# Kernel tuning notes

Measured on AMD Instinct MI355X. Metric: run time of the kernel, lower is better.

The kernel has to match this reference:

```python
import jax, jax.numpy as jnp
import numpy as np

B, PQ, C, NH, L, P, FF = 8, 900, 256, 8, 4, 4, 2048
SHAPES = [(100, 152), (50, 76), (25, 38), (13, 19)]
PK = sum(h * w for h, w in SHAPES)
DH = C // NH


def setup_inputs() -> dict:
    key = jax.random.key(0)
    ks = jax.random.split(key, 20)
    s = 0.02
    w = lambda i, shp: jax.random.normal(ks[i], shp, jnp.float32) * s
    starts = np.cumsum([0] + [h * wd for h, wd in SHAPES[:-1]]).astype(np.int64)
    return dict(
        query=w(0, (B, C, PQ)),
        key=w(1, (B, C, PK)),
        query_pos=jax.random.uniform(ks[2], (B, PQ, 3)),
        key_pos=jax.random.uniform(ks[3], (B, PK, 3)),
        reference_points=jax.random.uniform(ks[4], (B, PQ, L, 2)),
        W_in=w(5, (3 * C, C)), b_in=jnp.zeros(3 * C),
        W_out=w(6, (C, C)), b_out=jnp.zeros(C),
        W_off=w(7, (NH * L * P * 2, C)),
        b_off=jax.random.uniform(ks[8], (NH * L * P * 2,), minval=-1.0, maxval=1.0),
        W_aw=w(9, (NH * L * P, C)), b_aw=jnp.zeros(NH * L * P),
        W_v=w(10, (C, C)), b_v=jnp.zeros(C),
        W_o=w(11, (C, C)), b_o=jnp.zeros(C),
        W1=w(12, (FF, C)), b1=jnp.zeros(FF),
        W2=w(13, (C, FF)), b2=jnp.zeros(C),
        g1=jnp.ones(C), be1=jnp.zeros(C),
        g2=jnp.ones(C), be2=jnp.zeros(C),
        g3=jnp.ones(C), be3=jnp.zeros(C),
        spatial_shapes=np.array(SHAPES, np.int64),
        level_start_index=starts,
    )


def layer_norm(x, g, b):
    m = x.mean(-1, keepdims=True)
    v = x.var(-1, keepdims=True)
    return (x - m) * jax.lax.rsqrt(v + 1e-5) * g + b


def mha(x, W_in, b_in, W_out, b_out):
    # x: [S, B, C]; torch nn.MultiheadAttention with q=k=v=x
    S, Bn, _ = x.shape
    qkv = x @ W_in.T + b_in
    q, k, v = jnp.split(qkv, 3, axis=-1)
    to_h = lambda t: t.reshape(S, Bn, NH, DH).transpose(1, 2, 0, 3)  # [B,H,S,Dh]
    q, k, v = to_h(q), to_h(k), to_h(v)
    attn = jax.nn.softmax(jnp.einsum('bhqd,bhkd->bhqk', q, k) / np.sqrt(DH), axis=-1)
    o = jnp.einsum('bhqk,bhkd->bhqd', attn, v).transpose(2, 0, 1, 3).reshape(S, Bn, C)
    return o @ W_out.T + b_out


def ms_deform(value, loc, aw, shapes, starts):
    # value [B,PK,NH,DH], loc [B,PQ,NH,L,P,2] in [0,1], aw [B,PQ,NH,L,P]
    v = value.transpose(0, 2, 1, 3)          # [B,NH,PK,DH]
    locT = loc.transpose(0, 2, 1, 3, 4, 5)   # [B,NH,PQ,L,P,2]
    awT = aw.transpose(0, 2, 1, 3, 4)        # [B,NH,PQ,L,P]
    out = jnp.zeros((B, NH, PQ, DH), value.dtype)
    for l, (Hl, Wl) in enumerate(shapes):
        st = starts[l]
        vl = v[:, :, st:st + Hl * Wl]        # [B,NH,Hl*Wl,DH]
        x = locT[..., l, :, 0] * Wl - 0.5    # [B,NH,PQ,P]  (align_corners=False)
        y = locT[..., l, :, 1] * Hl - 0.5
        x0 = jnp.floor(x); y0 = jnp.floor(y)
        lw, lh = x - x0, y - y0
        x0i = x0.astype(jnp.int32); y0i = y0.astype(jnp.int32)

        def gather(ix, iy):
            valid = ((ix >= 0) & (ix < Wl) & (iy >= 0) & (iy < Hl)).astype(vl.dtype)
            idx = jnp.clip(iy, 0, Hl - 1) * Wl + jnp.clip(ix, 0, Wl - 1)
            g = jnp.take_along_axis(vl, idx.reshape(B, NH, -1, 1), axis=2)
            return g.reshape(B, NH, PQ, P, DH) * valid[..., None]

        samp = (gather(x0i, y0i) * ((1 - lw) * (1 - lh))[..., None]
                + gather(x0i + 1, y0i) * (lw * (1 - lh))[..., None]
                + gather(x0i, y0i + 1) * ((1 - lw) * lh)[..., None]
                + gather(x0i + 1, y0i + 1) * (lw * lh)[..., None])  # [B,NH,PQ,P,DH]
        out = out + (samp * awT[..., l, :, None]).sum(3)
    return out.transpose(0, 2, 1, 3).reshape(B, PQ, C)


def reference(query, key, query_pos, key_pos, reference_points,
              W_in, b_in, W_out, b_out, W_off, b_off, W_aw, b_aw,
              W_v, b_v, W_o, b_o, W1, b1, W2, b2,
              g1, be1, g2, be2, g3, be3,
              spatial_shapes, level_start_index):
    shapes = [tuple(int(t) for t in r) for r in np.asarray(spatial_shapes)]
    starts = [int(t) for t in np.asarray(level_start_index)]
    q = query.transpose(2, 0, 1)   # [PQ,B,C]
    k = key.transpose(2, 0, 1)     # [PK,B,C]
    # self-attention (posembeds are None in this config)
    q = layer_norm(q + mha(q, W_in, b_in, W_out, b_out), g1, be1)
    # multi-scale deformable cross-attention
    qd = q.transpose(1, 0, 2)      # [B,PQ,C]
    kf = k.transpose(1, 0, 2)      # [B,PK,C]
    value = (kf @ W_v.T + b_v).reshape(B, PK, NH, DH)
    off = (qd @ W_off.T + b_off).reshape(B, PQ, NH, L, P, 2)
    aw = jax.nn.softmax((qd @ W_aw.T + b_aw).reshape(B, PQ, NH, L * P), -1)
    aw = aw.reshape(B, PQ, NH, L, P)
    norm = jnp.asarray([[w_, h_] for (h_, w_) in shapes], jnp.float32)  # [L,2] as (W,H)
    loc = reference_points[:, :, None, :, None, :] + off / norm[None, None, None, :, None, :]
    q2 = ms_deform(value, loc, aw, shapes, starts) @ W_o.T + b_o
    q = layer_norm(q + q2.transpose(1, 0, 2), g2, be2)
    # FFN
    ff = jax.nn.relu(q @ W1.T + b1) @ W2.T + b2
    q = layer_norm(q + ff, g3, be3)
    return q.transpose(1, 2, 0)    # [B,C,PQ]
```

## Files before the change

kernel.cpp:

```cpp
#include <hip/hip_runtime.h>
#include <hip/hip_bf16.h>
#include <stdint.h>

typedef __hip_bfloat16 bf16;
typedef short bf16x8 __attribute__((ext_vector_type(8)));
typedef short s4v    __attribute__((ext_vector_type(4)));
typedef float f32x4  __attribute__((ext_vector_type(4)));

constexpr int B_  = 8;
constexpr int PQ_ = 900;
constexpr int C_  = 256;
constexpr int NH_ = 8;
constexpr int L_  = 4;
constexpr int P_  = 4;
constexpr int FF_ = 2048;
constexpr int DH_ = 32;
constexpr int PK_ = 20197;
constexpr int VLD = 960;

__device__ __forceinline__ short f2b(float f) {
    __hip_bfloat16 h = __float2bfloat16(f);
    union { __hip_bfloat16 h; short s; } u; u.h = h; return u.s;
}
__device__ __forceinline__ float b2f(short s) {
    union { short s; __hip_bfloat16 h; } u; u.s = s; return __bfloat162float(u.h);
}

template <int NF, bool DBUF, bool AF32, bool WF32, bool CF32, bool RELU>
__launch_bounds__(256)
__global__ void mfma_gemm(const void* __restrict__ Ap, const void* __restrict__ Wp,
                          const float* __restrict__ bias, void* __restrict__ Cp,
                          int Mb, int N, int K, int tilesM,
                          int ldA, int ldW, int ldC, int nbI,
                          int64_t sAo, int64_t sAi, int64_t sWo, int64_t sWi,
                          int64_t sCo, int64_t sCi, float scale)
{
    constexpr int BN  = 64 * NF;
    constexpr int LDR = 72;
    constexpr int NB  = DBUF ? 2 : 1;
    __shared__ short As[NB * 64 * LDR];
    __shared__ short Ws[NB * BN * LDR];

    const int tid   = threadIdx.x;
    const int batch = blockIdx.y / tilesM;
    const int m0    = (blockIdx.y % tilesM) * 64;
    const int n0    = blockIdx.x * BN;
    const int outer = batch / nbI, inner = batch % nbI;
    const int64_t offA = (int64_t)outer * sAo + (int64_t)inner * sAi;
    const int64_t offW = (int64_t)outer * sWo + (int64_t)inner * sWi;
    const int64_t offC = (int64_t)outer * sCo + (int64_t)inner * sCi;

    const int w = tid >> 6, lane = tid & 63;
    const int quad = lane >> 4, lrow = lane & 15;
    const int colbase = n0 + w * 16 * NF;

    const int sm  = tid >> 2;
    const int skb = (tid & 3) * 16;

    const int T = (K + 63) / 64;

    bf16x8 areg[2];
    bf16x8 wreg[2 * NF];

    auto stageA = [&](int t) {
        const int k0 = t * 64;
        const int gm = m0 + sm;
#pragma unroll
        for (int c = 0; c < 2; ++c) {
            const int k = k0 + skb + c * 8;
            bf16x8 pk = {0, 0, 0, 0, 0, 0, 0, 0};
            if (gm < Mb && k + 8 <= K) {
                if (AF32) {
                    const float* s = (const float*)Ap + offA + (int64_t)gm * ldA + k;
                    float4 u0 = *(const float4*)s;
                    float4 u1 = *(const float4*)(s + 4);
                    pk = (bf16x8){f2b(u0.x), f2b(u0.y), f2b(u0.z), f2b(u0.w),
                                  f2b(u1.x), f2b(u1.y), f2b(u1.z), f2b(u1.w)};
                } else {
                    pk = *(const bf16x8*)((const short*)Ap + offA + (int64_t)gm * ldA + k);
                }
            }
            areg[c] = pk;
        }
    };
    auto stageW = [&](int t) {
        const int k0 = t * 64;
#pragma unroll
        for (int j = 0; j < NF; ++j) {
            const int gn = n0 + j * 64 + sm;
#pragma unroll
            for (int c = 0; c < 2; ++c) {
                const int k = k0 + skb + c * 8;
                bf16x8 pk = {0, 0, 0, 0, 0, 0, 0, 0};
                if (gn < N && k + 8 <= K) {
                    if (WF32) {
                        const float* s = (const float*)Wp + offW + (int64_t)gn * ldW + k;
                        float4 u0 = *(const float4*)s;
                        float4 u1 = *(const float4*)(s + 4);
                        pk = (bf16x8){f2b(u0.x), f2b(u0.y), f2b(u0.z), f2b(u0.w),
                                      f2b(u1.x), f2b(u1.y), f2b(u1.z), f2b(u1.w)};
                    } else {
                        pk = *(const bf16x8*)((const short*)Wp + offW + (int64_t)gn * ldW + k);
                    }
                }
                wreg[j * 2 + c] = pk;
            }
        }
    };
    auto writeLDS = [&](int buf) {
#pragma unroll
        for (int c = 0; c < 2; ++c)
            *(bf16x8*)&As[(buf * 64 + sm) * LDR + skb + c * 8] = areg[c];
#pragma unroll
        for (int j = 0; j < NF; ++j)
#pragma unroll
            for (int c = 0; c < 2; ++c)
                *(bf16x8*)&Ws[(buf * BN + j * 64 + sm) * LDR + skb + c * 8] = wreg[j * 2 + c];
    };

    f32x4 acc[4][NF];
#pragma unroll
    for (int i = 0; i < 4; ++i)
#pragma unroll
        for (int j = 0; j < NF; ++j) acc[i][j] = (f32x4){0.f, 0.f, 0.f, 0.f};

    auto compute = [&](int buf) {
        bf16x8 a[4][2], bb[NF][2];
#pragma unroll
        for (int kh = 0; kh < 2; ++kh) {
#pragma unroll
            for (int mf = 0; mf < 4; ++mf)
                a[mf][kh] = *(const bf16x8*)&As[(buf * 64 + mf * 16 + lrow) * LDR + kh * 32 + quad * 8];
#pragma unroll
            for (int nf = 0; nf < NF; ++nf)
                bb[nf][kh] = *(const bf16x8*)&Ws[(buf * BN + w * 16 * NF + nf * 16 + lrow) * LDR + kh * 32 + quad * 8];
        }
#pragma unroll
        for (int kh = 0; kh < 2; ++kh)
#pragma unroll
            for (int mf = 0; mf < 4; ++mf)
#pragma unroll
                for (int nf = 0; nf < NF; ++nf)
                    acc[mf][nf] = __builtin_amdgcn_mfma_f32_16x16x32_bf16(a[mf][kh], bb[nf][kh], acc[mf][nf], 0, 0, 0);
    };

    if (DBUF) {
        stageA(0); stageW(0); writeLDS(0);
        __syncthreads();
        for (int t = 0; t < T; ++t) {
            const int cur = t & 1;
            if (t + 1 < T) { stageA(t + 1); stageW(t + 1); }
            compute(cur);
            if (t + 1 < T) {
                writeLDS(cur ^ 1);
                __syncthreads();
            }
        }
    } else {
        for (int t = 0; t < T; ++t) {
            stageA(t); stageW(t);
            if (t > 0) __syncthreads();
            writeLDS(0);
            __syncthreads();
            compute(0);
        }
    }

#pragma unroll
    for (int nf = 0; nf < NF; ++nf) {
        const int col = colbase + nf * 16 + lrow;
        if (col >= N) continue;
        const float bia = bias ? bias[col] : 0.f;
#pragma unroll
        for (int mf = 0; mf < 4; ++mf) {
            const int row0 = m0 + mf * 16 + quad * 4;
#pragma unroll
            for (int r = 0; r < 4; ++r) {
                const int rr = row0 + r;
                if (rr < Mb) {
                    float v = acc[mf][nf][r] * scale + bia;
                    if (RELU) v = fmaxf(v, 0.f);
                    const int64_t idx = offC + (int64_t)rr * ldC + col;
                    if (CF32) ((float*)Cp)[idx] = v;
                    else      ((short*)Cp)[idx] = f2b(v);
                }
            }
        }
    }
}

template <int NF, bool DBUF, bool AF32, bool WF32, bool CF32, bool RELU>
static void mfma_launch(const void* A, const void* W, const float* bias, void* Cp,
                        int nb, int nbI, int Mb, int N, int K,
                        int ldA, int ldW, int ldC,
                        int64_t sAo, int64_t sAi, int64_t sWo, int64_t sWi,
                        int64_t sCo, int64_t sCi, float scale, hipStream_t stream)
{
    int tilesM = (Mb + 63) / 64;
    dim3 grid((N + 64 * NF - 1) / (64 * NF), nb * tilesM);
    mfma_gemm<NF, DBUF, AF32, WF32, CF32, RELU><<<grid, 256, 0, stream>>>(
        A, W, bias, Cp, Mb, N, K, tilesM, ldA, ldW, ldC, nbI,
        sAo, sAi, sWo, sWi, sCo, sCi, scale);
}

__launch_bounds__(256)
__global__ void transpose_kernel(const float* __restrict__ src, short* __restrict__ dst,
                                 int Scount, int ldS, int64_t sbs, int64_t dbs)
{
    const int tid = threadIdx.x;
    const int b = blockIdx.z;
    const int s0 = blockIdx.x * 32, c0 = blockIdx.y * 32;
    __shared__ float t[32][33];
    {
        const int c_l = tid >> 3, sq = (tid & 7) * 4;
        const int64_t base = (int64_t)b * sbs + (int64_t)(c0 + c_l) * ldS;
#pragma unroll
        for (int i = 0; i < 4; ++i) {
            const int s = s0 + sq + i;
            t[c_l][sq + i] = (s < Scount) ? src[base + s] : 0.f;
        }
    }
    __syncthreads();
    {
        const int s_l = tid >> 3, cq = (tid & 7) * 4;
        const int s = s0 + s_l;
        if (s < Scount) {
            s4v pk = {f2b(t[cq + 0][s_l]), f2b(t[cq + 1][s_l]),
                      f2b(t[cq + 2][s_l]), f2b(t[cq + 3][s_l])};
            *(s4v*)&dst[(int64_t)b * dbs + (int64_t)s * 256 + c0 + cq] = pk;
        }
    }
}

__launch_bounds__(256)
__global__ void vt_kernel(const short* __restrict__ qkv, short* __restrict__ VT)
{
    const int tid = threadIdx.x;
    const int bh = blockIdx.y, b = bh >> 3, h = bh & 7;
    const int s0 = blockIdx.x * 32;
    __shared__ short t[32][36];
    {
        const int s_l = tid >> 3, dq = (tid & 7) * 4;
        const int s = s0 + s_l;
        s4v pk = {0, 0, 0, 0};
        if (s < 900)
            pk = *(const s4v*)&qkv[((int64_t)(b * 900 + s)) * 768 + 512 + h * 32 + dq];
        *(s4v*)&t[s_l][dq] = pk;
    }
    __syncthreads();
    {
        const int d = tid >> 3, sq = (tid & 7) * 4;
        s4v pk = {t[sq + 0][d], t[sq + 1][d], t[sq + 2][d], t[sq + 3][d]};
        *(s4v*)&VT[((int64_t)bh * 32 + d) * VLD + s0 + sq] = pk;
    }
}

__launch_bounds__(256)
__global__ void attn_fused(const short* __restrict__ qkv, const short* __restrict__ VT,
                           short* __restrict__ attno)
{
    __shared__ short Pl[4 * 16 * 72];
    const int tid = threadIdx.x;
    const int wv = tid >> 6, lane = tid & 63;
    const int quad = lane >> 4, lrow = lane & 15;
    const int bh = blockIdx.y, b = bh >> 3, h = bh & 7;
    const int q0 = blockIdx.x * 64 + wv * 16;
    const float iscale = 0.17677669529663687f;

    bf16x8 aq = {0, 0, 0, 0, 0, 0, 0, 0};
    {
        const int q = q0 + lrow;
        if (q < 900)
            aq = *(const bf16x8*)&qkv[((int64_t)(b * 900 + q)) * 768 + h * 32 + quad * 8];
    }

    float mrow[4], lsum[4];
    f32x4 o[2] = {{0.f, 0.f, 0.f, 0.f}, {0.f, 0.f, 0.f, 0.f}};
#pragma unroll
    for (int r = 0; r < 4; ++r) { mrow[r] = -1e30f; lsum[r] = 0.f; }

    short* Pw = &Pl[wv * 16 * 72];

    for (int st = 0; st < 15; ++st) {
        const int s0 = st * 64;
        f32x4 sc[4];
#pragma unroll
        for (int nf = 0; nf < 4; ++nf) {
            const int s = s0 + nf * 16 + lrow;
            bf16x8 kb = {0, 0, 0, 0, 0, 0, 0, 0};
            if (s < 900)
                kb = *(const bf16x8*)&qkv[((int64_t)(b * 900 + s)) * 768 + 256 + h * 32 + quad * 8];
            sc[nf] = __builtin_amdgcn_mfma_f32_16x16x32_bf16(aq, kb, (f32x4){0.f, 0.f, 0.f, 0.f}, 0, 0, 0);
        }
#pragma unroll
        for (int nf = 0; nf < 4; ++nf) {
            const int s = s0 + nf * 16 + lrow;
            if (s >= 900) sc[nf] = (f32x4){-1e30f, -1e30f, -1e30f, -1e30f};
            else {
#pragma unroll
                for (int r = 0; r < 4; ++r) sc[nf][r] *= iscale;
            }
        }
        float alpha[4], ps[4][4], rsum[4];
#pragma unroll
        for (int r = 0; r < 4; ++r) {
            float tm = fmaxf(fmaxf(sc[0][r], sc[1][r]), fmaxf(sc[2][r], sc[3][r]));
#pragma unroll
            for (int off = 1; off < 16; off <<= 1)
                tm = fmaxf(tm, __shfl_xor(tm, off, 64));
            const float nm = fmaxf(mrow[r], tm);
            alpha[r] = __expf(mrow[r] - nm);
            mrow[r] = nm;
            float s4 = 0.f;
#pragma unroll
            for (int nf = 0; nf < 4; ++nf) {
                const float p = __expf(sc[nf][r] - nm);
                ps[nf][r] = p;
                s4 += p;
            }
#pragma unroll
            for (int off = 1; off < 16; off <<= 1)
                s4 += __shfl_xor(s4, off, 64);
            rsum[r] = s4;
        }
#pragma unroll
        for (int nf2 = 0; nf2 < 2; ++nf2)
#pragma unroll
            for (int r = 0; r < 4; ++r) o[nf2][r] *= alpha[r];
#pragma unroll
        for (int r = 0; r < 4; ++r) lsum[r] = lsum[r] * alpha[r] + rsum[r];
#pragma unroll
        for (int nf = 0; nf < 4; ++nf)
#pragma unroll
            for (int r = 0; r < 4; ++r)
                Pw[(quad * 4 + r) * 72 + nf * 16 + lrow] = f2b(ps[nf][r]);
#pragma unroll
        for (int kh = 0; kh < 2; ++kh) {
            bf16x8 pa = *(const bf16x8*)&Pw[lrow * 72 + kh * 32 + quad * 8];
#pragma unroll
            for (int nf2 = 0; nf2 < 2; ++nf2) {
                const int d = nf2 * 16 + lrow;
                bf16x8 vb = *(const bf16x8*)&VT[((int64_t)bh * 32 + d) * VLD + s0 + kh * 32 + quad * 8];
                o[nf2] = __builtin_amdgcn_mfma_f32_16x16x32_bf16(pa, vb, o[nf2], 0, 0, 0);
            }
        }
    }
#pragma unroll
    for (int r = 0; r < 4; ++r) {
        const int q = q0 + quad * 4 + r;
        if (q < 900) {
            const float inv = 1.f / lsum[r];
#pragma unroll
            for (int nf2 = 0; nf2 < 2; ++nf2)
                attno[((int64_t)(b * 900 + q)) * 256 + h * 32 + nf2 * 16 + lrow] = f2b(o[nf2][r] * inv);
        }
    }
}

template <int MODE>
__launch_bounds__(256)
__global__ void ln_kernel(const float* __restrict__ y, const void* __restrict__ res,
                          const float* __restrict__ g, const float* __restrict__ be,
                          float* __restrict__ out_f, short* __restrict__ out_b)
{
    const int bt = blockIdx.x;
    const int b = bt / PQ_, t = bt % PQ_;
    const int c = threadIdx.x;

    float r;
    if (MODE == 0)      r = ((const float*)res)[((int64_t)b * C_ + c) * PQ_ + t];
    else if (MODE == 1) r = ((const float*)res)[(int64_t)bt * C_ + c];
    else                r = b2f(((const short*)res)[(int64_t)bt * C_ + c]);
    const float v = r + y[(int64_t)bt * C_ + c];

    __shared__ float s1[256], s2[256];
    s1[c] = v; s2[c] = v * v;
    __syncthreads();
    for (int st = 128; st > 0; st >>= 1) {
        if (c < st) { s1[c] += s1[c + st]; s2[c] += s2[c + st]; }
        __syncthreads();
    }
    const float mean = s1[0] * (1.f / C_);
    const float var  = s2[0] * (1.f / C_) - mean * mean;
    const float o = (v - mean) * rsqrtf(var + 1e-5f) * g[c] + be[c];

    if (MODE == 0) { out_f[(int64_t)bt * C_ + c] = o; out_b[(int64_t)bt * C_ + c] = f2b(o); }
    else if (MODE == 1) out_b[(int64_t)bt * C_ + c] = f2b(o);
    else out_f[((int64_t)b * C_ + c) * PQ_ + t] = o;
}

__launch_bounds__(256)
__global__ void deform_kernel(const float* __restrict__ offb, const float* __restrict__ awl,
                              const float* __restrict__ refp, const short* __restrict__ value,
                              short* __restrict__ samp)
{
    const int bt = blockIdx.x;
    const int b = bt / PQ_;
    const int tid = threadIdx.x;
    const int h = tid >> 5, d = tid & 31;

    __shared__ float Loff[256];
    __shared__ float Law[128];
    __shared__ float Lref[8];

    Loff[tid] = offb[(int64_t)bt * 256 + tid];
    if (tid < 128) Law[tid] = awl[(int64_t)bt * 128 + tid];
    if (tid < 8)   Lref[tid] = refp[(int64_t)bt * 8 + tid];
    __syncthreads();

    float m = -1e30f;
#pragma unroll
    for (int i = 0; i < 16; ++i) m = fmaxf(m, Law[h * 16 + i]);
    float s = 0.f;
#pragma unroll
    for (int i = 0; i < 16; ++i) s += __expf(Law[h * 16 + i] - m);
    const float invs = 1.f / s;

    const int HLc[4] = {100, 50, 25, 13};
    const int WLc[4] = {152, 76, 38, 19};
    const int STc[4] = {0, 15200, 19000, 19950};

    float acc = 0.f;
#pragma unroll
    for (int l = 0; l < L_; ++l) {
        const int Hl = HLc[l], Wl = WLc[l], st0 = STc[l];
        const float fx = Lref[l * 2 + 0], fy = Lref[l * 2 + 1];
#pragma unroll
        for (int p = 0; p < P_; ++p) {
            const float ox = Loff[h * 32 + l * 8 + p * 2 + 0];
            const float oy = Loff[h * 32 + l * 8 + p * 2 + 1];
            const float x = (fx + ox / (float)Wl) * (float)Wl - 0.5f;
            const float y = (fy + oy / (float)Hl) * (float)Hl - 0.5f;
            const float x0f = floorf(x), y0f = floorf(y);
            const int x0 = (int)x0f, y0 = (int)y0f;
            const float lw = x - x0f, lh = y - y0f;
            const float w00 = (1.f - lw) * (1.f - lh), w10 = lw * (1.f - lh);
            const float w01 = (1.f - lw) * lh,         w11 = lw * lh;
            const float aww = __expf(Law[h * 16 + l * 4 + p] - m) * invs;

            float sv = 0.f;
            int ix, iy; float w;
#pragma unroll
            for (int cidx = 0; cidx < 4; ++cidx) {
                if (cidx == 0) { ix = x0;     iy = y0;     w = w00; }
                if (cidx == 1) { ix = x0 + 1; iy = y0;     w = w10; }
                if (cidx == 2) { ix = x0;     iy = y0 + 1; w = w01; }
                if (cidx == 3) { ix = x0 + 1; iy = y0 + 1; w = w11; }
                if (ix >= 0 && ix < Wl && iy >= 0 && iy < Hl) {
                    const int64_t vi = ((int64_t)(b * PK_ + st0 + iy * Wl + ix)) * 256 + h * 32 + d;
                    sv += w * b2f(value[vi]);
                }
            }
            acc += sv * aww;
        }
    }
    samp[(int64_t)bt * 256 + tid] = f2b(acc);
}

extern "C" void kernel_launch(void* const* d_in, const int* in_sizes, int n_in,
                              void* d_out, int out_size, void* d_ws, size_t ws_size,
                              hipStream_t stream)
{
    const float* query = (const float*)d_in[0];
    const float* key   = (const float*)d_in[1];
    const float* refp  = (const float*)d_in[4];
    const float* W_in  = (const float*)d_in[5];
    const float* b_in  = (const float*)d_in[6];
    const float* W_out = (const float*)d_in[7];
    const float* b_out = (const float*)d_in[8];
    const float* W_off = (const float*)d_in[9];
    const float* b_off = (const float*)d_in[10];
    const float* W_aw  = (const float*)d_in[11];
    const float* b_aw  = (const float*)d_in[12];
    const float* W_v   = (const float*)d_in[13];
    const float* b_v   = (const float*)d_in[14];
    const float* W_o   = (const float*)d_in[15];
    const float* b_o   = (const float*)d_in[16];
    const float* W1    = (const float*)d_in[17];
    const float* b1    = (const float*)d_in[18];
    const float* W2    = (const float*)d_in[19];
    const float* b2    = (const float*)d_in[20];
    const float* g1    = (const float*)d_in[21];
    const float* be1   = (const float*)d_in[22];
    const float* g2    = (const float*)d_in[23];
    const float* be2   = (const float*)d_in[24];
    const float* g3    = (const float*)d_in[25];
    const float* be3   = (const float*)d_in[26];

    char* X  = (char*)d_ws;
    char* Yb = X + 62259200;
    char* Z1 = Yb + 7372800;
    char* Wa = Z1 + 7372800;
    char* Wb = Wa + 3686400;
    char* KT = Wb + 3686400;
    char* VA = KT + 82726912;

    short* qkvb   = (short*)X;
    short* queryT = (short*)(X + 11059200);
    short* VT     = (short*)(X + 14745600);
    short* attno  = (short*)(X + 18677760);
    short* ffh    = (short*)X;
    float* proj   = (float*)Yb;
    float* offb   = (float*)Yb;
    float* proj2  = (float*)Yb;
    float* ffo    = (float*)Yb;
    float* q1     = (float*)Z1;
    short* q1b    = (short*)Wa;
    short* samp   = (short*)Wa;
    float* awl    = (float*)Wb;
    short* q2nb   = (short*)Wb;
    short* keyT   = (short*)KT;
    short* value  = (short*)VA;

    transpose_kernel<<<dim3(29, 8, B_), 256, 0, stream>>>(query, queryT, PQ_, PQ_,
                                                          (int64_t)C_ * PQ_, (int64_t)PQ_ * C_);
    mfma_launch<1, true, false, true, false, false>(queryT, W_in, b_in, qkvb, 1, 1, B_ * PQ_, 768, 256,
                                                    256, 256, 768, 0, 0, 0, 0, 0, 0, 1.f, stream);
    vt_kernel<<<dim3(30, 64), 256, 0, stream>>>(qkvb, VT);
    attn_fused<<<dim3(15, 64), 256, 0, stream>>>(qkvb, VT, attno);
    mfma_launch<1, true, false, true, true, false>(attno, W_out, b_out, proj, 1, 1, B_ * PQ_, 256, 256,
                                                   256, 256, 256, 0, 0, 0, 0, 0, 0, 1.f, stream);
    ln_kernel<0><<<B_ * PQ_, 256, 0, stream>>>(proj, query, g1, be1, q1, q1b);
    mfma_launch<1, true, false, true, true, false>(q1b, W_off, b_off, offb, 1, 1, B_ * PQ_, 256, 256,
                                                   256, 256, 256, 0, 0, 0, 0, 0, 0, 1.f, stream);
    mfma_launch<1, true, false, true, true, false>(q1b, W_aw, b_aw, awl, 1, 1, B_ * PQ_, 128, 256,
                                                   256, 256, 128, 0, 0, 0, 0, 0, 0, 1.f, stream);
    transpose_kernel<<<dim3((PK_ + 31) / 32, 8, B_), 256, 0, stream>>>(
        key, keyT, PK_, PK_, (int64_t)C_ * PK_, (int64_t)PK_ * 256);
    mfma_launch<1, true, false, true, false, false>(keyT, W_v, b_v, value, 1, 1, B_ * PK_, 256, 256,
                                                    256, 256, 256, 0, 0, 0, 0, 0, 0, 1.f, stream);
    deform_kernel<<<B_ * PQ_, 256, 0, stream>>>(offb, awl, refp, value, samp);
    mfma_launch<1, true, false, true, true, false>(samp, W_o, b_o, proj2, 1, 1, B_ * PQ_, 256, 256,
                                                   256, 256, 256, 0, 0, 0, 0, 0, 0, 1.f, stream);
    ln_kernel<1><<<B_ * PQ_, 256, 0, stream>>>(proj2, q1, g2, be2, nullptr, q2nb);
    mfma_launch<1, true, false, true, false, true>(q2nb, W1, b1, ffh, 1, 1, B_ * PQ_, FF_, 256,
                                                   256, 256, FF_, 0, 0, 0, 0, 0, 0, 1.f, stream);
    mfma_launch<1, true, false, true, true, false>(ffh, W2, b2, ffo, 1, 1, B_ * PQ_, 256, FF_,
                                                   FF_, FF_, 256, 0, 0, 0, 0, 0, 0, 1.f, stream);
    ln_kernel<2><<<B_ * PQ_, 256, 0, stream>>>(ffo, q2nb, g3, be3, (float*)d_out, nullptr);

    (void)in_sizes; (void)n_in; (void)out_size; (void)ws_size;
}
```

Baseline: 774.6 us.

## Pre-convert weights to bf16 and add a weight-resident value projection kernel

```diff
diff --git a/kernel.cpp b/kernel.cpp
--- a/kernel.cpp
+++ b/kernel.cpp
@@ -24,6 +24,28 @@
 }
 __device__ __forceinline__ float b2f(short s) {
     union { short s; __hip_bfloat16 h; } u; u.s = s; return __bfloat162float(u.h);
+}
+
+__launch_bounds__(256)
+__global__ void wcvt_kernel(const float* __restrict__ p0, const float* __restrict__ p1,
+                            const float* __restrict__ p2, const float* __restrict__ p3,
+                            const float* __restrict__ p4, const float* __restrict__ p5,
+                            const float* __restrict__ p6, const float* __restrict__ p7,
+                            short* __restrict__ dst)
+{
+    const int g = (blockIdx.x * 256 + threadIdx.x) * 4;
+    const float* src; int off;
+    if      (g < 196608)  { src = p0; off = 0; }
+    else if (g < 262144)  { src = p1; off = 196608; }
+    else if (g < 327680)  { src = p2; off = 262144; }
+    else if (g < 360448)  { src = p3; off = 327680; }
+    else if (g < 425984)  { src = p4; off = 360448; }
+    else if (g < 491520)  { src = p5; off = 425984; }
+    else if (g < 1015808) { src = p6; off = 491520; }
+    else                  { src = p7; off = 1015808; }
+    float4 v = *(const float4*)(src + (g - off));
+    s4v pk = {f2b(v.x), f2b(v.y), f2b(v.z), f2b(v.w)};
+    *(s4v*)&dst[g] = pk;
 }
 
 template <int NF, bool DBUF, bool AF32, bool WF32, bool CF32, bool RELU>
@@ -201,6 +223,85 @@
     mfma_gemm<NF, DBUF, AF32, WF32, CF32, RELU><<<grid, 256, 0, stream>>>(
         A, W, bias, Cp, Mb, N, K, tilesM, ldA, ldW, ldC, nbI,
         sAo, sAi, sWo, sWi, sCo, sCi, scale);
+}
+
+__launch_bounds__(256)
+__global__ void vproj_kernel(const short* __restrict__ A, const short* __restrict__ Wb,
+                             const float* __restrict__ bias, short* __restrict__ Cp,
+                             int Mb, int nTiles)
+{
+    __shared__ short Ws[128 * 256];
+    const int tid = threadIdx.x;
+    const int n0 = blockIdx.x * 128;
+    const int w = tid >> 6, lane = tid & 63;
+    const int quad = lane >> 4, lrow = lane & 15;
+
+    {
+        const int n = tid >> 1, hk = tid & 1;
+        const int64_t src = (int64_t)(n0 + n) * 256 + hk * 128;
+#pragma unroll
+        for (int j = 0; j < 16; ++j) {
+            const int slot = hk * 16 + j;
+            bf16x8 pk = *(const bf16x8*)&Wb[src + j * 8];
+            *(bf16x8*)((char*)Ws + n * 512 + ((slot ^ (n & 7)) << 4)) = pk;
+        }
+    }
+    __syncthreads();
+
+    const int nbase = w * 32;
+    float bia[2];
+#pragma unroll
+    for (int nf = 0; nf < 2; ++nf) bia[nf] = bias[n0 + nbase + nf * 16 + lrow];
+
+    for (int it = 0; it < 4; ++it) {
+        const int ti = blockIdx.y * 4 + it;
+        if (ti >= nTiles) break;
+        const int m0 = ti * 64;
+
+        f32x4 acc[4][2];
+#pragma unroll
+        for (int mf = 0; mf < 4; ++mf)
+#pragma unroll
+            for (int nf = 0; nf < 2; ++nf) acc[mf][nf] = (f32x4){0.f, 0.f, 0.f, 0.f};
+
+#pragma unroll
+        for (int kh = 0; kh < 8; ++kh) {
+            bf16x8 a[4];
+#pragma unroll
+            for (int mf = 0; mf < 4; ++mf) {
+                const int gm = m0 + mf * 16 + lrow;
+                a[mf] = (gm < Mb)
+                    ? *(const bf16x8*)&A[(int64_t)gm * 256 + kh * 32 + quad * 8]
+                    : (bf16x8){0, 0, 0, 0, 0, 0, 0, 0};
+            }
+            bf16x8 b[2];
+#pragma unroll
+            for (int nf = 0; nf < 2; ++nf) {
+                const int n = nbase + nf * 16 + lrow;
+                b[nf] = *(const bf16x8*)((const char*)Ws + n * 512 +
+                                         ((((kh << 2) | quad) ^ (lrow & 7)) << 4));
+            }
+#pragma unroll
+            for (int mf = 0; mf < 4; ++mf)
+#pragma unroll
+                for (int nf = 0; nf < 2; ++nf)
+                    acc[mf][nf] = __builtin_amdgcn_mfma_f32_16x16x32_bf16(a[mf], b[nf], acc[mf][nf], 0, 0, 0);
+        }
+
+#pragma unroll
+        for (int nf = 0; nf < 2; ++nf) {
+            const int col = n0 + nbase + nf * 16 + lrow;
+#pragma unroll
+            for (int mf = 0; mf < 4; ++mf) {
+#pragma unroll
+                for (int r = 0; r < 4; ++r) {
+                    const int rr = m0 + mf * 16 + quad * 4 + r;
+                    if (rr < Mb)
+                        Cp[(int64_t)rr * 256 + col] = f2b(acc[mf][nf][r] + bia[nf]);
+                }
+            }
+        }
+    }
 }
 
 __launch_bounds__(256)
@@ -491,9 +592,10 @@
     char* Yb = X + 62259200;
     char* Z1 = Yb + 7372800;
     char* Wa = Z1 + 7372800;
-    char* Wb = Wa + 3686400;
-    char* KT = Wb + 3686400;
+    char* Wb_ = Wa + 3686400;
+    char* KT = Wb_ + 3686400;
     char* VA = KT + 82726912;
+    char* WB = VA + 82726912;
 
     short* qkvb   = (short*)X;
     short* queryT = (short*)(X + 11059200);
@@ -507,36 +609,50 @@
     float* q1     = (float*)Z1;
     short* q1b    = (short*)Wa;
     short* samp   = (short*)Wa;
-    float* awl    = (float*)Wb;
-    short* q2nb   = (short*)Wb;
+    float* awl    = (float*)Wb_;
+    short* q2nb   = (short*)Wb_;
     short* keyT   = (short*)KT;
     short* value  = (short*)VA;
 
+    short* WBs    = (short*)WB;
+    short* Wb_in  = WBs;
+    short* Wb_out = WBs + 196608;
+    short* Wb_off = WBs + 262144;
+    short* Wb_aw  = WBs + 327680;
+    short* Wb_v   = WBs + 360448;
+    short* Wb_o   = WBs + 425984;
+    short* Wb1    = WBs + 491520;
+    short* Wb2    = WBs + 1015808;
+
+    wcvt_kernel<<<1504, 256, 0, stream>>>(W_in, W_out, W_off, W_aw, W_v, W_o, W1, W2, WBs);
     transpose_kernel<<<dim3(29, 8, B_), 256, 0, stream>>>(query, queryT, PQ_, PQ_,
                                                           (int64_t)C_ * PQ_, (int64_t)PQ_ * C_);
-    mfma_launch<1, true, false, true, false, false>(queryT, W_in, b_in, qkvb, 1, 1, B_ * PQ_, 768, 256,
-                                                    256, 256, 768, 0, 0, 0, 0, 0, 0, 1.f, stream);
+    mfma_launch<1, true, false, false, false, false>(queryT, Wb_in, b_in, qkvb, 1, 1, B_ * PQ_, 768, 256,
+                                                     256, 256, 768, 0, 0, 0, 0, 0, 0, 1.f, stream);
     vt_kernel<<<dim3(30, 64), 256, 0, stream>>>(qkvb, VT);
     attn_fused<<<dim3(15, 64), 256, 0, stream>>>(qkvb, VT, attno);
-    mfma_launch<1, true, false, true, true, false>(attno, W_out, b_out, proj, 1, 1, B_ * PQ_, 256, 256,
-                                                   256, 256, 256, 0, 0, 0, 0, 0, 0, 1.f, stream);
+    mfma_launch<1, true, false, false, true, false>(attno, Wb_out, b_out, proj, 1, 1, B_ * PQ_, 256, 256,
+                                                    256, 256, 256, 0, 0, 0, 0, 0, 0, 1.f, stream);
     ln_kernel<0><<<B_ * PQ_, 256, 0, stream>>>(proj, query, g1, be1, q1, q1b);
-    mfma_launch<1, true, false, true, true, false>(q1b, W_off, b_off, offb, 1, 1, B_ * PQ_, 256, 256,
-                                                   256, 256, 256, 0, 0, 0, 0, 0, 0, 1.f, stream);
-    mfma_launch<1, true, false, true, true, false>(q1b, W_aw, b_aw, awl, 1, 1, B_ * PQ_, 128, 256,
-                                                   256, 256, 128, 0, 0, 0, 0, 0, 0, 1.f, stream);
+    mfma_launch<1, true, false, false, true, false>(q1b, Wb_off, b_off, offb, 1, 1, B_ * PQ_, 256, 256,
+                                                    256, 256, 256, 0, 0, 0, 0, 0, 0, 1.f, stream);
+    mfma_launch<1, true, false, false, true, false>(q1b, Wb_aw, b_aw, awl, 1, 1, B_ * PQ_, 128, 256,
+                                                    256, 256, 128, 0, 0, 0, 0, 0, 0, 1.f, stream);
     transpose_kernel<<<dim3((PK_ + 31) / 32, 8, B_), 256, 0, stream>>>(
         key, keyT, PK_, PK_, (int64_t)C_ * PK_, (int64_t)PK_ * 256);
-    mfma_launch<1, true, false, true, false, false>(keyT, W_v, b_v, value, 1, 1, B_ * PK_, 256, 256,
+    {
+        const int nTiles = (B_ * PK_ + 63) / 64;
+        vproj_kernel<<<dim3(2, (nTiles + 3) / 4), 256, 0, stream>>>(
+            keyT, Wb_v, b_v, value, B_ * PK_, nTiles);
+    }
+    deform_kernel<<<B_ * PQ_, 256, 0, stream>>>(offb, awl, refp, value, samp);
+    mfma_launch<1, true, false, false, true, false>(samp, Wb_o, b_o, proj2, 1, 1, B_ * PQ_, 256, 256,
                                                     256, 256, 256, 0, 0, 0, 0, 0, 0, 1.f, stream);
-    deform_kernel<<<B_ * PQ_, 256, 0, stream>>>(offb, awl, refp, value, samp);
-    mfma_launch<1, true, false, true, true, false>(samp, W_o, b_o, proj2, 1, 1, B_ * PQ_, 256, 256,
-                                                   256, 256, 256, 0, 0, 0, 0, 0, 0, 1.f, stream);
     ln_kernel<1><<<B_ * PQ_, 256, 0, stream>>>(proj2, q1, g2, be2, nullptr, q2nb);
-    mfma_launch<1, true, false, true, false, true>(q2nb, W1, b1, ffh, 1, 1, B_ * PQ_, FF_, 256,
-                                                   256, 256, FF_, 0, 0, 0, 0, 0, 0, 1.f, stream);
-    mfma_launch<1, true, false, true, true, false>(ffh, W2, b2, ffo, 1, 1, B_ * PQ_, 256, FF_,
-                                                   FF_, FF_, 256, 0, 0, 0, 0, 0, 0, 1.f, stream);
+    mfma_launch<1, true, false, false, false, true>(q2nb, Wb1, b1, ffh, 1, 1, B_ * PQ_, FF_, 256,
+                                                    256, 256, FF_, 0, 0, 0, 0, 0, 0, 1.f, stream);
+    mfma_launch<1, true, false, false, true, false>(ffh, Wb2, b2, ffo, 1, 1, B_ * PQ_, 256, FF_,
+                                                    FF_, FF_, 256, 0, 0, 0, 0, 0, 0, 1.f, stream);
     ln_kernel<2><<<B_ * PQ_, 256, 0, stream>>>(ffo, q2nb, g3, be3, (float*)d_out, nullptr);
 
     (void)in_sizes; (void)n_in; (void)out_size; (void)ws_size;
```

Result: faster. 739.2 us (-4.6%).
